# Kernel tuning notes

Hardware: AMD Instinct MI355X
Metric: run time of the kernel (lower is better)

The kernel has to match this reference:

```python
import jax, jax.numpy as jnp
import numpy as np

L = 4          # num_layers
DIM = 256      # model dim
HEADS = 8
DH = DIM // HEADS
WINDOW = 512   # sliding window size
FF = 4 * DIM
EPS = 1e-5


def setup_inputs() -> dict:
    key = jax.random.key(0)
    ks = jax.random.split(key, 13)
    B, S = 1, 4096
    s = 0.02
    inp = {
        "x": jax.random.normal(ks[0], (B, S, DIM), jnp.float32),
        # per-layer stacked weights (leading axis = layer) for lax.scan
        "wq": jax.random.normal(ks[1], (L, DIM, DIM), jnp.float32) * s,
        "bq": jnp.zeros((L, DIM), jnp.float32),
        "wk": jax.random.normal(ks[2], (L, DIM, DIM), jnp.float32) * s,
        "bk": jnp.zeros((L, DIM), jnp.float32),
        "wv": jax.random.normal(ks[3], (L, DIM, DIM), jnp.float32) * s,
        "bv": jnp.zeros((L, DIM), jnp.float32),
        "wo": jax.random.normal(ks[4], (L, DIM, DIM), jnp.float32) * s,
        "bo": jnp.zeros((L, DIM), jnp.float32),
        "w1": jax.random.normal(ks[5], (L, DIM, FF), jnp.float32) * s,
        "b1": jnp.zeros((L, FF), jnp.float32),
        "w2": jax.random.normal(ks[6], (L, FF, DIM), jnp.float32) * s,
        "b2": jnp.zeros((L, DIM), jnp.float32),
    }
    return inp


def _ln(x):
    # LayerNorm with elementwise_affine=False
    m = jnp.mean(x, axis=-1, keepdims=True)
    v = jnp.var(x, axis=-1, keepdims=True)
    return (x - m) / jnp.sqrt(v + EPS)


def reference(x, wq, bq, wk, bk, wv, bv, wo, bo, w1, b1, w2, b2):
    B, S, D = x.shape
    idx = jnp.arange(S)
    # sliding window mask: |q_idx - kv_idx| <= window_size // 2
    mask = jnp.abs(idx[:, None] - idx[None, :]) <= (WINDOW // 2)  # [S, S]
    neg = jnp.finfo(x.dtype).min
    scale = 1.0 / np.sqrt(DH)

    def layer(h, p):
        lwq, lbq, lwk, lbk, lwv, lbv, lwo, lbo, lw1, lb1, lw2, lb2 = p
        # pre-norm self-attention residual
        n = _ln(h)
        q = (n @ lwq + lbq).reshape(B, S, HEADS, DH)
        k = (n @ lwk + lbk).reshape(B, S, HEADS, DH)
        v = (n @ lwv + lbv).reshape(B, S, HEADS, DH)
        scores = jnp.einsum('bqhd,bkhd->bhqk', q, k) * scale
        scores = jnp.where(mask, scores, neg)
        attn = jax.nn.softmax(scores, axis=-1)
        o = jnp.einsum('bhqk,bkhd->bqhd', attn, v).reshape(B, S, D)
        h = h + o @ lwo + lbo
        # post-norm dense residual: x = norm(x); x = x + ffn(x)
        h = _ln(h)
        h = h + jax.nn.gelu(h @ lw1 + lb1) @ lw2 + lb2
        return h, None

    x, _ = jax.lax.scan(layer, x, (wq, bq, wk, bk, wv, bv, wo, bo, w1, b1, w2, b2))
    return x
```

## Files before the change

### kernel.cpp

```cpp
#include <hip/hip_runtime.h>
#include <math.h>

#define SEQ 4096
#define DIM 256
#define NH 8
#define DHD 32
#define FFD 1024
#define NLAYER 4

typedef unsigned short ushort_t;
typedef __attribute__((ext_vector_type(8))) short bf16x8;
typedef __attribute__((ext_vector_type(4))) float f32x4;

__device__ __forceinline__ float gelu_f(float x){
  const float c = 0.7978845608028654f;
  float x3 = x*x*x;
  return 0.5f * x * (1.0f + tanhf(c*(x + 0.044715f*x3)));
}

__device__ __forceinline__ ushort_t f2b(float f){
  union { float f; unsigned u; } x; x.f = f;
  unsigned r = x.u + 0x7FFF + ((x.u >> 16) & 1);
  return (ushort_t)(r >> 16);
}

__device__ __forceinline__ void gload16(void* lds, const void* g){
  __builtin_amdgcn_global_load_lds((const __attribute__((address_space(1))) void*)g,
                                   (__attribute__((address_space(3))) void*)lds, 16, 0, 0);
}

__global__ __launch_bounds__(256) void wconv_kernel(
    const float* __restrict__ wq, const float* __restrict__ wk,
    const float* __restrict__ wv, const float* __restrict__ wo,
    const float* __restrict__ w1, const float* __restrict__ w2,
    ushort_t* __restrict__ wt){
  __shared__ ushort_t tile[64][65];
  int b = blockIdx.x, tid = threadIdx.x;
  const float* src; ushort_t* dst; int K, N, tk, tn;
  if (b < 256){
    int m = b>>6, rem = b&63, l = rem>>4, t = rem&15;
    K = 256; N = 256; tk = t>>2; tn = t&3;
    const float* s4 = (m==0)?wq:(m==1)?wk:(m==2)?wv:wo;
    src = s4 + (size_t)l*65536;
    dst = wt + (size_t)(m*NLAYER + l)*65536;
  } else if (b < 512){
    int rem = b-256, l = rem>>6, t = rem&63;
    K = 256; N = 1024; tk = t>>4; tn = t&15;
    src = w1 + (size_t)l*262144;
    dst = wt + 1048576 + (size_t)l*262144;
  } else {
    int rem = b-512, l = rem>>6, t = rem&63;
    K = 1024; N = 256; tk = t>>2; tn = t&3;
    src = w2 + (size_t)l*262144;
    dst = wt + 2097152 + (size_t)l*262144;
  }
  int k0 = tk*64, n0 = tn*64;
  #pragma unroll
  for (int i=0;i<16;i++){
    int idx = tid + 256*i, row = idx>>6, col = idx&63;
    tile[row][col] = f2b(src[(size_t)(k0+row)*N + n0+col]);
  }
  __syncthreads();
  #pragma unroll
  for (int i=0;i<16;i++){
    int idx = tid + 256*i, nrow = idx>>6, kcol = idx&63;
    dst[(size_t)(n0+nrow)*K + k0+kcol] = tile[kcol][nrow];
  }
}

__global__ __launch_bounds__(256) void ln_kernel(const float* __restrict__ x,
    float* __restrict__ yf, ushort_t* __restrict__ yb){
  int row  = blockIdx.x*4 + (threadIdx.x>>6);
  int lane = threadIdx.x & 63;
  const float4* xr = (const float4*)(x + (size_t)row*DIM);
  float4 v = xr[lane];
  float s  = v.x+v.y+v.z+v.w;
  float sq = v.x*v.x+v.y*v.y+v.z*v.z+v.w*v.w;
  #pragma unroll
  for(int off=32; off>0; off>>=1){
    s  += __shfl_down(s, off);
    sq += __shfl_down(sq, off);
  }
  s = __shfl(s, 0); sq = __shfl(sq, 0);
  float mean = s * (1.0f/DIM);
  float var  = sq * (1.0f/DIM) - mean*mean;
  float rinv = rsqrtf(var + 1e-5f);
  float4 o;
  o.x=(v.x-mean)*rinv; o.y=(v.y-mean)*rinv; o.z=(v.z-mean)*rinv; o.w=(v.w-mean)*rinv;
  if (yf) ((float4*)(yf + (size_t)row*DIM))[lane] = o;
  if (yb){
    ushort_t* yp = yb + (size_t)row*DIM + lane*4;
    yp[0]=f2b(o.x); yp[1]=f2b(o.y); yp[2]=f2b(o.z); yp[3]=f2b(o.w);
  }
}

__global__ __launch_bounds__(256) void gemm_kernel(
    const ushort_t* __restrict__ A, const ushort_t* __restrict__ Wt,
    const float* __restrict__ bias, const float* __restrict__ R,
    float* __restrict__ Cf, ushort_t* __restrict__ Cb,
    int M, int N, int K, int act){
  __shared__ ushort_t As[32*256];
  __shared__ ushort_t Bs[64*256];
  int tid = threadIdx.x;
  int w = tid>>6, lane = tid&63;
  int wr = w>>1, wc = w&1;
  int q4 = lane>>4, u = lane&15;
  int m0 = blockIdx.y*32, n0 = blockIdx.x*64;
  f32x4 acc[2];
  acc[0] = (f32x4){0.f,0.f,0.f,0.f};
  acc[1] = (f32x4){0.f,0.f,0.f,0.f};

  for (int k0 = 0; k0 < K; k0 += 256){
    if (k0) __syncthreads();
    #pragma unroll
    for (int i=0;i<4;i++){
      int idx = tid + 256*i;
      int row = idx>>5, ch = idx&31;
      gload16(&As[idx*8], &A[(size_t)(m0+row)*K + k0 + ((ch^(row&7))*8)]);
    }
    #pragma unroll
    for (int i=0;i<8;i++){
      int idx = tid + 256*i;
      int row = idx>>5, ch = idx&31;
      gload16(&Bs[idx*8], &Wt[(size_t)(n0+row)*K + k0 + ((ch^(row&7))*8)]);
    }
    __syncthreads();
    #pragma unroll
    for (int kk=0;kk<8;kk++){
      int ar = wr*16 + u;
      bf16x8 af = *(const bf16x8*)&As[ar*256 + (((kk*4+q4)^(ar&7))*8)];
      #pragma unroll
      for (int j=0;j<2;j++){
        int br = wc*32 + j*16 + u;
        bf16x8 bf = *(const bf16x8*)&Bs[br*256 + (((kk*4+q4)^(br&7))*8)];
        acc[j] = __builtin_amdgcn_mfma_f32_16x16x32_bf16(af, bf, acc[j], 0, 0, 0);
      }
    }
  }
  #pragma unroll
  for (int j=0;j<2;j++){
    #pragma unroll
    for (int t=0;t<4;t++){
      int m = m0 + wr*16 + q4*4 + t;
      int n = n0 + wc*32 + j*16 + u;
      float val = acc[j][t] + bias[n];
      if (R)   val += R[(size_t)m*N + n];
      if (act) val = gelu_f(val);
      if (Cf)  Cf[(size_t)m*N + n] = val;
      if (Cb)  Cb[(size_t)m*N + n] = f2b(val);
    }
  }
}

__global__ __launch_bounds__(256) void qkv_kernel(
    const float* __restrict__ hin,
    const ushort_t* __restrict__ wtq, const ushort_t* __restrict__ wtk, const ushort_t* __restrict__ wtv,
    const float* __restrict__ bqp, const float* __restrict__ bkp, const float* __restrict__ bvp,
    ushort_t* __restrict__ qo, ushort_t* __restrict__ ko, ushort_t* __restrict__ vo){
  __shared__ ushort_t As[32*256];
  __shared__ ushort_t Bs[64*256];
  int tid = threadIdx.x;
  int w = tid>>6, lane = tid&63;
  int wr = w>>1, wc = w&1;
  int q4 = lane>>4, u = lane&15;
  int m0 = blockIdx.y*32, n0 = blockIdx.x*64;
  int z = blockIdx.z;
  const ushort_t* Wt = (z==0)?wtq:(z==1)?wtk:wtv;
  const float* bias  = (z==0)?bqp:(z==1)?bkp:bvp;
  ushort_t* Cb       = (z==0)?qo :(z==1)?ko :vo;

  #pragma unroll
  for (int i=0;i<8;i++){
    int idx = tid + 256*i;
    int row = idx>>5, ch = idx&31;
    gload16(&Bs[idx*8], &Wt[(size_t)(n0+row)*DIM + ((ch^(row&7))*8)]);
  }
  #pragma unroll
  for (int r=0;r<8;r++){
    int row = w*8 + r;
    float4 v = *(const float4*)&hin[(size_t)(m0+row)*DIM + lane*4];
    float s  = v.x+v.y+v.z+v.w;
    float sq = v.x*v.x+v.y*v.y+v.z*v.z+v.w*v.w;
    #pragma unroll
    for (int off=32; off>0; off>>=1){ s += __shfl_down(s,off); sq += __shfl_down(sq,off); }
    s = __shfl(s,0); sq = __shfl(sq,0);
    float mean = s*(1.0f/DIM), var = sq*(1.0f/DIM) - mean*mean;
    float rinv = rsqrtf(var + 1e-5f);
    int ch = lane>>1, half = lane&1;
    ushort4 o4;
    o4.x = f2b((v.x-mean)*rinv); o4.y = f2b((v.y-mean)*rinv);
    o4.z = f2b((v.z-mean)*rinv); o4.w = f2b((v.w-mean)*rinv);
    *(ushort4*)&As[row*256 + ((ch^(row&7))*8 + half*4)] = o4;
  }
  __syncthreads();

  f32x4 acc[2];
  acc[0] = (f32x4){0.f,0.f,0.f,0.f};
  acc[1] = (f32x4){0.f,0.f,0.f,0.f};
  #pragma unroll
  for (int kk=0;kk<8;kk++){
    int ar = wr*16 + u;
    bf16x8 af = *(const bf16x8*)&As[ar*256 + (((kk*4+q4)^(ar&7))*8)];
    #pragma unroll
    for (int j=0;j<2;j++){
      int br = wc*32 + j*16 + u;
      bf16x8 bf = *(const bf16x8*)&Bs[br*256 + (((kk*4+q4)^(br&7))*8)];
      acc[j] = __builtin_amdgcn_mfma_f32_16x16x32_bf16(af, bf, acc[j], 0, 0, 0);
    }
  }
  #pragma unroll
  for (int j=0;j<2;j++){
    #pragma unroll
    for (int t=0;t<4;t++){
      int m = m0 + wr*16 + q4*4 + t;
      int n = n0 + wc*32 + j*16 + u;
      Cb[(size_t)m*DIM + n] = f2b(acc[j][t] + bias[n]);
    }
  }
}

__global__ __launch_bounds__(256) void attn_kernel(
    const ushort_t* __restrict__ q, const ushort_t* __restrict__ k,
    const ushort_t* __restrict__ v, ushort_t* __restrict__ out){
  int q0 = blockIdx.x * 64;
  int h  = blockIdx.y;
  int tid = threadIdx.x;
  int w = tid >> 6;
  int lane = tid & 63;
  int u = lane & 15, q4 = lane >> 4;

  __shared__ ushort_t Ks[64][40];
  __shared__ ushort_t Vt[32][72];
  __shared__ ushort_t Pw[4][16][72];

  bf16x8 aq = *(const bf16x8*)(q + (size_t)(q0 + w*16 + u)*DIM + h*DHD + q4*8);

  float m[4], l[4];
  f32x4 acc[2];
  #pragma unroll
  for (int t=0;t<4;t++){ m[t] = -INFINITY; l[t] = 0.f; }
  acc[0] = (f32x4){0.f,0.f,0.f,0.f};
  acc[1] = (f32x4){0.f,0.f,0.f,0.f};

  const float sl2 = 0.25510703448358519f;

  int lo = q0 - 256; if (lo < 0) lo = 0;
  int hi = q0 + 63 + 256; if (hi > SEQ-1) hi = SEQ-1;
  int kt1 = (hi >> 6) << 6;

  for (int kt = (lo >> 6) << 6; kt <= kt1; kt += 64){
    __syncthreads();
    {
      int key = tid >> 2, d0 = (tid & 3) * 8;
      bf16x8 kv = *(const bf16x8*)(k + (size_t)(kt+key)*DIM + h*DHD + d0);
      *(bf16x8*)&Ks[key][d0] = kv;
      int vd0 = w * 8;
      bf16x8 vv = *(const bf16x8*)(v + (size_t)(kt+lane)*DIM + h*DHD + vd0);
      #pragma unroll
      for (int j=0;j<8;j++) Vt[vd0+j][lane] = (ushort_t)vv[j];
    }
    __syncthreads();

    f32x4 sc[4];
    #pragma unroll
    for (int t4=0;t4<4;t4++){
      bf16x8 bk = *(const bf16x8*)&Ks[t4*16 + u][q4*8];
      sc[t4] = __builtin_amdgcn_mfma_f32_16x16x32_bf16(aq, bk, (f32x4){0.f,0.f,0.f,0.f}, 0, 0, 0);
    }

    bool needs_mask = (kt < q0-192) || (kt > q0+192);
    #pragma unroll
    for (int t=0;t<4;t++){
      float mx = -INFINITY;
      if (needs_mask){
        int q_idx = q0 + w*16 + q4*4 + t;
        #pragma unroll
        for (int t4=0;t4<4;t4++){
          float s = sc[t4][t] * sl2;
          int k_idx = kt + t4*16 + u;
          int diff = q_idx - k_idx; if (diff < 0) diff = -diff;
          if (diff > 256) s = -INFINITY;
          sc[t4][t] = s;
          mx = fmaxf(mx, s);
        }
      } else {
        #pragma unroll
        for (int t4=0;t4<4;t4++){
          float s = sc[t4][t] * sl2;
          sc[t4][t] = s;
          mx = fmaxf(mx, s);
        }
      }
      mx = fmaxf(mx, __shfl_xor(mx, 1));
      mx = fmaxf(mx, __shfl_xor(mx, 2));
      mx = fmaxf(mx, __shfl_xor(mx, 4));
      mx = fmaxf(mx, __shfl_xor(mx, 8));
      float nm = fmaxf(m[t], mx);
      float al = exp2f(m[t] - nm);
      float rs = 0.f;
      #pragma unroll
      for (int t4=0;t4<4;t4++){
        float p = exp2f(sc[t4][t] - nm);
        rs += p;
        Pw[w][q4*4+t][t4*16+u] = f2b(p);
      }
      rs += __shfl_xor(rs, 1);
      rs += __shfl_xor(rs, 2);
      rs += __shfl_xor(rs, 4);
      rs += __shfl_xor(rs, 8);
      l[t] = l[t]*al + rs;
      m[t] = nm;
      acc[0][t] *= al;
      acc[1][t] *= al;
    }
    #pragma unroll
    for (int kk=0;kk<2;kk++){
      bf16x8 ap = *(const bf16x8*)&Pw[w][u][kk*32 + q4*8];
      #pragma unroll
      for (int d=0; d<2; d++){
        bf16x8 bvf = *(const bf16x8*)&Vt[d*16 + u][kk*32 + q4*8];
        acc[d] = __builtin_amdgcn_mfma_f32_16x16x32_bf16(ap, bvf, acc[d], 0, 0, 0);
      }
    }
  }

  float rl[4];
  #pragma unroll
  for (int t=0;t<4;t++) rl[t] = 1.0f / l[t];
  #pragma unroll
  for (int d=0; d<2; d++)
    #pragma unroll
    for (int t=0;t<4;t++)
      out[(size_t)(q0 + w*16 + q4*4 + t)*DIM + h*DHD + d*16 + u] = f2b(acc[d][t]*rl[t]);
}

extern "C" void kernel_launch(void* const* d_in, const int* in_sizes, int n_in,
                              void* d_out, int out_size, void* d_ws, size_t ws_size,
                              hipStream_t stream) {
  const float* x  = (const float*)d_in[0];
  const float* wq = (const float*)d_in[1];
  const float* bq = (const float*)d_in[2];
  const float* wk = (const float*)d_in[3];
  const float* bk = (const float*)d_in[4];
  const float* wv = (const float*)d_in[5];
  const float* bv = (const float*)d_in[6];
  const float* wo = (const float*)d_in[7];
  const float* bo = (const float*)d_in[8];
  const float* w1 = (const float*)d_in[9];
  const float* b1 = (const float*)d_in[10];
  const float* w2 = (const float*)d_in[11];
  const float* b2 = (const float*)d_in[12];
  float* out = (float*)d_out;
  float* ws  = (float*)d_ws;

  ushort_t* wt    = (ushort_t*)ws;
  ushort_t* abuf  = (ushort_t*)(ws + 1572864);
  ushort_t* ffbf  = (ushort_t*)(ws + 2097152);
  float* qb = ws + 4194304;
  float* kb = ws + 5242880;
  float* vb = ws + 6291456;
  float* hb = ws + 7340032;
  ushort_t* qbh = (ushort_t*)qb;
  ushort_t* kbh = (ushort_t*)kb;
  ushort_t* vbh = (ushort_t*)vb;

  const ushort_t* w1t_base = wt + 1048576;
  const ushort_t* w2t_base = wt + 2097152;

  const dim3 blk(256);
  wconv_kernel<<<768, blk, 0, stream>>>(wq, wk, wv, wo, w1, w2, wt);

  for (int l = 0; l < NLAYER; l++){
    const float* hin = (l == 0) ? x : hb;
    const ushort_t* lwq = wt + (size_t)(0*NLAYER + l)*65536;
    const ushort_t* lwk = wt + (size_t)(1*NLAYER + l)*65536;
    const ushort_t* lwv = wt + (size_t)(2*NLAYER + l)*65536;
    const ushort_t* lwo = wt + (size_t)(3*NLAYER + l)*65536;
    const ushort_t* lw1 = w1t_base + (size_t)l*262144;
    const ushort_t* lw2 = w2t_base + (size_t)l*262144;

    qkv_kernel<<<dim3(4,128,3), blk, 0, stream>>>(hin, lwq, lwk, lwv,
        bq + (size_t)l*DIM, bk + (size_t)l*DIM, bv + (size_t)l*DIM, qbh, kbh, vbh);
    attn_kernel<<<dim3(SEQ/64, NH), blk, 0, stream>>>(qbh, kbh, vbh, abuf);
    gemm_kernel<<<dim3(4,128), blk, 0, stream>>>(abuf, lwo, bo + (size_t)l*DIM,
        hin, qb, nullptr, SEQ, DIM, DIM, 0);
    ln_kernel<<<SEQ/4, blk, 0, stream>>>(qb, kb, abuf);
    gemm_kernel<<<dim3(16,128), blk, 0, stream>>>(abuf, lw1, b1 + (size_t)l*FFD,
        nullptr, nullptr, ffbf, SEQ, FFD, DIM, 1);
    float* hout = (l == NLAYER-1) ? out : hb;
    gemm_kernel<<<dim3(4,128), blk, 0, stream>>>(ffbf, lw2, b2 + (size_t)l*DIM,
        kb, hout, nullptr, SEQ, DIM, FFD, 0);
  }
}
```

Measured before the change: 381.0 us.

## Enlarge GEMM M-tile, fuse QKV per block, double-buffer attention K/V tiles

The GEMM and QKV kernels now compute 64x64 output tiles with a 2x2 MFMA accumulator block per wave, which halves the grid and improves register-level reuse of the A and B fragments. The QKV kernel computes the LayerNorm once per block and loops over the Q, K and V weights, reloading the B tile into shared memory between them instead of launching three z-slices. The attention kernel double-buffers its K/V shared tiles, prefetching the next tile into registers during compute and dropping one barrier per iteration. In exchange the kernels use more LDS and registers and launch fewer blocks, which may reduce occupancy and parallelism.

```diff
diff --git a/kernel.cpp b/kernel.cpp
--- a/kernel.cpp
+++ b/kernel.cpp
@@ -99,21 +99,24 @@
     const float* __restrict__ bias, const float* __restrict__ R,
     float* __restrict__ Cf, ushort_t* __restrict__ Cb,
     int M, int N, int K, int act){
-  __shared__ ushort_t As[32*256];
+  __shared__ ushort_t As[64*256];
   __shared__ ushort_t Bs[64*256];
   int tid = threadIdx.x;
   int w = tid>>6, lane = tid&63;
   int wr = w>>1, wc = w&1;
   int q4 = lane>>4, u = lane&15;
-  int m0 = blockIdx.y*32, n0 = blockIdx.x*64;
-  f32x4 acc[2];
-  acc[0] = (f32x4){0.f,0.f,0.f,0.f};
-  acc[1] = (f32x4){0.f,0.f,0.f,0.f};
+  int m0 = blockIdx.y*64, n0 = blockIdx.x*64;
+  f32x4 acc[2][2];
+  #pragma unroll
+  for (int i=0;i<2;i++)
+    #pragma unroll
+    for (int j=0;j<2;j++)
+      acc[i][j] = (f32x4){0.f,0.f,0.f,0.f};
 
   for (int k0 = 0; k0 < K; k0 += 256){
     if (k0) __syncthreads();
     #pragma unroll
-    for (int i=0;i<4;i++){
+    for (int i=0;i<8;i++){
       int idx = tid + 256*i;
       int row = idx>>5, ch = idx&31;
       gload16(&As[idx*8], &A[(size_t)(m0+row)*K + k0 + ((ch^(row&7))*8)]);
@@ -127,27 +130,38 @@
     __syncthreads();
     #pragma unroll
     for (int kk=0;kk<8;kk++){
-      int ar = wr*16 + u;
-      bf16x8 af = *(const bf16x8*)&As[ar*256 + (((kk*4+q4)^(ar&7))*8)];
+      bf16x8 af[2], bf[2];
+      #pragma unroll
+      for (int i=0;i<2;i++){
+        int ar = wr*32 + i*16 + u;
+        af[i] = *(const bf16x8*)&As[ar*256 + (((kk*4+q4)^(ar&7))*8)];
+      }
       #pragma unroll
       for (int j=0;j<2;j++){
         int br = wc*32 + j*16 + u;
-        bf16x8 bf = *(const bf16x8*)&Bs[br*256 + (((kk*4+q4)^(br&7))*8)];
-        acc[j] = __builtin_amdgcn_mfma_f32_16x16x32_bf16(af, bf, acc[j], 0, 0, 0);
-      }
-    }
-  }
-  #pragma unroll
-  for (int j=0;j<2;j++){
-    #pragma unroll
-    for (int t=0;t<4;t++){
-      int m = m0 + wr*16 + q4*4 + t;
-      int n = n0 + wc*32 + j*16 + u;
-      float val = acc[j][t] + bias[n];
-      if (R)   val += R[(size_t)m*N + n];
-      if (act) val = gelu_f(val);
-      if (Cf)  Cf[(size_t)m*N + n] = val;
-      if (Cb)  Cb[(size_t)m*N + n] = f2b(val);
+        bf[j] = *(const bf16x8*)&Bs[br*256 + (((kk*4+q4)^(br&7))*8)];
+      }
+      #pragma unroll
+      for (int i=0;i<2;i++)
+        #pragma unroll
+        for (int j=0;j<2;j++)
+          acc[i][j] = __builtin_amdgcn_mfma_f32_16x16x32_bf16(af[i], bf[j], acc[i][j], 0, 0, 0);
+    }
+  }
+  #pragma unroll
+  for (int i=0;i<2;i++){
+    #pragma unroll
+    for (int j=0;j<2;j++){
+      #pragma unroll
+      for (int t=0;t<4;t++){
+        int m = m0 + wr*32 + i*16 + q4*4 + t;
+        int n = n0 + wc*32 + j*16 + u;
+        float val = acc[i][j][t] + bias[n];
+        if (R)   val += R[(size_t)m*N + n];
+        if (act) val = gelu_f(val);
+        if (Cf)  Cf[(size_t)m*N + n] = val;
+        if (Cb)  Cb[(size_t)m*N + n] = f2b(val);
+      }
     }
   }
 }
@@ -157,27 +171,23 @@
     const ushort_t* __restrict__ wtq, const ushort_t* __restrict__ wtk, const ushort_t* __restrict__ wtv,
     const float* __restrict__ bqp, const float* __restrict__ bkp, const float* __restrict__ bvp,
     ushort_t* __restrict__ qo, ushort_t* __restrict__ ko, ushort_t* __restrict__ vo){
-  __shared__ ushort_t As[32*256];
+  __shared__ ushort_t As[64*256];
   __shared__ ushort_t Bs[64*256];
   int tid = threadIdx.x;
   int w = tid>>6, lane = tid&63;
   int wr = w>>1, wc = w&1;
   int q4 = lane>>4, u = lane&15;
-  int m0 = blockIdx.y*32, n0 = blockIdx.x*64;
-  int z = blockIdx.z;
-  const ushort_t* Wt = (z==0)?wtq:(z==1)?wtk:wtv;
-  const float* bias  = (z==0)?bqp:(z==1)?bkp:bvp;
-  ushort_t* Cb       = (z==0)?qo :(z==1)?ko :vo;
+  int m0 = blockIdx.y*64, n0 = blockIdx.x*64;
 
   #pragma unroll
   for (int i=0;i<8;i++){
     int idx = tid + 256*i;
     int row = idx>>5, ch = idx&31;
-    gload16(&Bs[idx*8], &Wt[(size_t)(n0+row)*DIM + ((ch^(row&7))*8)]);
-  }
-  #pragma unroll
-  for (int r=0;r<8;r++){
-    int row = w*8 + r;
+    gload16(&Bs[idx*8], &wtq[(size_t)(n0+row)*DIM + ((ch^(row&7))*8)]);
+  }
+  #pragma unroll
+  for (int r=0;r<16;r++){
+    int row = w*16 + r;
     float4 v = *(const float4*)&hin[(size_t)(m0+row)*DIM + lane*4];
     float s  = v.x+v.y+v.z+v.w;
     float sq = v.x*v.x+v.y*v.y+v.z*v.z+v.w*v.w;
@@ -194,28 +204,56 @@
   }
   __syncthreads();
 
-  f32x4 acc[2];
-  acc[0] = (f32x4){0.f,0.f,0.f,0.f};
-  acc[1] = (f32x4){0.f,0.f,0.f,0.f};
-  #pragma unroll
-  for (int kk=0;kk<8;kk++){
-    int ar = wr*16 + u;
-    bf16x8 af = *(const bf16x8*)&As[ar*256 + (((kk*4+q4)^(ar&7))*8)];
-    #pragma unroll
-    for (int j=0;j<2;j++){
-      int br = wc*32 + j*16 + u;
-      bf16x8 bf = *(const bf16x8*)&Bs[br*256 + (((kk*4+q4)^(br&7))*8)];
-      acc[j] = __builtin_amdgcn_mfma_f32_16x16x32_bf16(af, bf, acc[j], 0, 0, 0);
-    }
-  }
-  #pragma unroll
-  for (int j=0;j<2;j++){
-    #pragma unroll
-    for (int t=0;t<4;t++){
-      int m = m0 + wr*16 + q4*4 + t;
-      int n = n0 + wc*32 + j*16 + u;
-      Cb[(size_t)m*DIM + n] = f2b(acc[j][t] + bias[n]);
-    }
+  #pragma unroll
+  for (int z=0; z<3; z++){
+    const float* bias = (z==0)?bqp:(z==1)?bkp:bvp;
+    ushort_t* Cb      = (z==0)?qo :(z==1)?ko :vo;
+    f32x4 acc[2][2];
+    #pragma unroll
+    for (int i=0;i<2;i++)
+      #pragma unroll
+      for (int j=0;j<2;j++)
+        acc[i][j] = (f32x4){0.f,0.f,0.f,0.f};
+    #pragma unroll
+    for (int kk=0;kk<8;kk++){
+      bf16x8 af[2], bf[2];
+      #pragma unroll
+      for (int i=0;i<2;i++){
+        int ar = wr*32 + i*16 + u;
+        af[i] = *(const bf16x8*)&As[ar*256 + (((kk*4+q4)^(ar&7))*8)];
+      }
+      #pragma unroll
+      for (int j=0;j<2;j++){
+        int br = wc*32 + j*16 + u;
+        bf[j] = *(const bf16x8*)&Bs[br*256 + (((kk*4+q4)^(br&7))*8)];
+      }
+      #pragma unroll
+      for (int i=0;i<2;i++)
+        #pragma unroll
+        for (int j=0;j<2;j++)
+          acc[i][j] = __builtin_amdgcn_mfma_f32_16x16x32_bf16(af[i], bf[j], acc[i][j], 0, 0, 0);
+    }
+    if (z < 2){
+      __syncthreads();
+      const ushort_t* Wn = (z==0)?wtk:wtv;
+      #pragma unroll
+      for (int i=0;i<8;i++){
+        int idx = tid + 256*i;
+        int row = idx>>5, ch = idx&31;
+        gload16(&Bs[idx*8], &Wn[(size_t)(n0+row)*DIM + ((ch^(row&7))*8)]);
+      }
+    }
+    #pragma unroll
+    for (int i=0;i<2;i++)
+      #pragma unroll
+      for (int j=0;j<2;j++)
+        #pragma unroll
+        for (int t=0;t<4;t++){
+          int m = m0 + wr*32 + i*16 + q4*4 + t;
+          int n = n0 + wc*32 + j*16 + u;
+          Cb[(size_t)m*DIM + n] = f2b(acc[i][j][t] + bias[n]);
+        }
+    if (z < 2) __syncthreads();
   }
 }
 
@@ -229,8 +267,8 @@
   int lane = tid & 63;
   int u = lane & 15, q4 = lane >> 4;
 
-  __shared__ ushort_t Ks[64][40];
-  __shared__ ushort_t Vt[32][72];
+  __shared__ ushort_t Ks[2][64][40];
+  __shared__ ushort_t Vt[2][32][72];
   __shared__ ushort_t Pw[4][16][72];
 
   bf16x8 aq = *(const bf16x8*)(q + (size_t)(q0 + w*16 + u)*DIM + h*DHD + q4*8);
@@ -246,25 +284,31 @@
 
   int lo = q0 - 256; if (lo < 0) lo = 0;
   int hi = q0 + 63 + 256; if (hi > SEQ-1) hi = SEQ-1;
+  int kt0 = (lo >> 6) << 6;
   int kt1 = (hi >> 6) << 6;
 
-  for (int kt = (lo >> 6) << 6; kt <= kt1; kt += 64){
+  int key = tid >> 2, d0 = (tid & 3) * 8;
+  int vd0 = w * 8;
+
+  bf16x8 kr = *(const bf16x8*)(k + (size_t)(kt0+key)*DIM + h*DHD + d0);
+  bf16x8 vr = *(const bf16x8*)(v + (size_t)(kt0+lane)*DIM + h*DHD + vd0);
+  *(bf16x8*)&Ks[0][key][d0] = kr;
+  #pragma unroll
+  for (int j=0;j<8;j++) Vt[0][vd0+j][lane] = (ushort_t)vr[j];
+
+  int p = 0;
+  for (int kt = kt0; kt <= kt1; kt += 64, p ^= 1){
     __syncthreads();
-    {
-      int key = tid >> 2, d0 = (tid & 3) * 8;
-      bf16x8 kv = *(const bf16x8*)(k + (size_t)(kt+key)*DIM + h*DHD + d0);
-      *(bf16x8*)&Ks[key][d0] = kv;
-      int vd0 = w * 8;
-      bf16x8 vv = *(const bf16x8*)(v + (size_t)(kt+lane)*DIM + h*DHD + vd0);
-      #pragma unroll
-      for (int j=0;j<8;j++) Vt[vd0+j][lane] = (ushort_t)vv[j];
-    }
-    __syncthreads();
+    bool have_next = (kt + 64 <= kt1);
+    if (have_next){
+      kr = *(const bf16x8*)(k + (size_t)(kt+64+key)*DIM + h*DHD + d0);
+      vr = *(const bf16x8*)(v + (size_t)(kt+64+lane)*DIM + h*DHD + vd0);
+    }
 
     f32x4 sc[4];
     #pragma unroll
     for (int t4=0;t4<4;t4++){
-      bf16x8 bk = *(const bf16x8*)&Ks[t4*16 + u][q4*8];
+      bf16x8 bk = *(const bf16x8*)&Ks[p][t4*16 + u][q4*8];
       sc[t4] = __builtin_amdgcn_mfma_f32_16x16x32_bf16(aq, bk, (f32x4){0.f,0.f,0.f,0.f}, 0, 0, 0);
     }
 
@@ -300,9 +344,9 @@
       float rs = 0.f;
       #pragma unroll
       for (int t4=0;t4<4;t4++){
-        float p = exp2f(sc[t4][t] - nm);
-        rs += p;
-        Pw[w][q4*4+t][t4*16+u] = f2b(p);
+        float pv = exp2f(sc[t4][t] - nm);
+        rs += pv;
+        Pw[w][q4*4+t][t4*16+u] = f2b(pv);
       }
       rs += __shfl_xor(rs, 1);
       rs += __shfl_xor(rs, 2);
@@ -318,9 +362,14 @@
       bf16x8 ap = *(const bf16x8*)&Pw[w][u][kk*32 + q4*8];
       #pragma unroll
       for (int d=0; d<2; d++){
-        bf16x8 bvf = *(const bf16x8*)&Vt[d*16 + u][kk*32 + q4*8];
+        bf16x8 bvf = *(const bf16x8*)&Vt[p][d*16 + u][kk*32 + q4*8];
         acc[d] = __builtin_amdgcn_mfma_f32_16x16x32_bf16(ap, bvf, acc[d], 0, 0, 0);
       }
+    }
+    if (have_next){
+      *(bf16x8*)&Ks[p^1][key][d0] = kr;
+      #pragma unroll
+      for (int j=0;j<8;j++) Vt[p^1][vd0+j][lane] = (ushort_t)vr[j];
     }
   }
 
@@ -379,16 +428,16 @@
     const ushort_t* lw1 = w1t_base + (size_t)l*262144;
     const ushort_t* lw2 = w2t_base + (size_t)l*262144;
 
-    qkv_kernel<<<dim3(4,128,3), blk, 0, stream>>>(hin, lwq, lwk, lwv,
+    qkv_kernel<<<dim3(4,64), blk, 0, stream>>>(hin, lwq, lwk, lwv,
         bq + (size_t)l*DIM, bk + (size_t)l*DIM, bv + (size_t)l*DIM, qbh, kbh, vbh);
     attn_kernel<<<dim3(SEQ/64, NH), blk, 0, stream>>>(qbh, kbh, vbh, abuf);
-    gemm_kernel<<<dim3(4,128), blk, 0, stream>>>(abuf, lwo, bo + (size_t)l*DIM,
+    gemm_kernel<<<dim3(4,64), blk, 0, stream>>>(abuf, lwo, bo + (size_t)l*DIM,
         hin, qb, nullptr, SEQ, DIM, DIM, 0);
     ln_kernel<<<SEQ/4, blk, 0, stream>>>(qb, kb, abuf);
-    gemm_kernel<<<dim3(16,128), blk, 0, stream>>>(abuf, lw1, b1 + (size_t)l*FFD,
+    gemm_kernel<<<dim3(16,64), blk, 0, stream>>>(abuf, lw1, b1 + (size_t)l*FFD,
         nullptr, nullptr, ffbf, SEQ, FFD, DIM, 1);
     float* hout = (l == NLAYER-1) ? out : hb;
-    gemm_kernel<<<dim3(4,128), blk, 0, stream>>>(ffbf, lw2, b2 + (size_t)l*DIM,
+    gemm_kernel<<<dim3(4,64), blk, 0, stream>>>(ffbf, lw2, b2 + (size_t)l*DIM,
         kb, hout, nullptr, SEQ, DIM, FFD, 0);
   }
 }
```

New measurement: 385.7 us. Within noise of the previous version (+1.2%).

## Reuse normalized A tile across Q/K/V and double-buffer K/V tiles in attention

Applied to the files above, without the earlier changes.

The QKV kernel now computes the LayerNorm'd activation tile once per block and loops over the three weight matrices, reloading only the B tile, instead of launching three z-slices that each redo the LN. The attention kernel double-buffers K and V in shared memory, prefetching the next tile into registers while computing on the current one, which removes one barrier per iteration. The cost is fewer QKV blocks (less parallelism), extra serialized weight loads within each block, and more shared memory in attention, which may lower occupancy.

```diff
diff --git a/kernel.cpp b/kernel.cpp
--- a/kernel.cpp
+++ b/kernel.cpp
@@ -164,16 +164,12 @@
   int wr = w>>1, wc = w&1;
   int q4 = lane>>4, u = lane&15;
   int m0 = blockIdx.y*32, n0 = blockIdx.x*64;
-  int z = blockIdx.z;
-  const ushort_t* Wt = (z==0)?wtq:(z==1)?wtk:wtv;
-  const float* bias  = (z==0)?bqp:(z==1)?bkp:bvp;
-  ushort_t* Cb       = (z==0)?qo :(z==1)?ko :vo;
 
   #pragma unroll
   for (int i=0;i<8;i++){
     int idx = tid + 256*i;
     int row = idx>>5, ch = idx&31;
-    gload16(&Bs[idx*8], &Wt[(size_t)(n0+row)*DIM + ((ch^(row&7))*8)]);
+    gload16(&Bs[idx*8], &wtq[(size_t)(n0+row)*DIM + ((ch^(row&7))*8)]);
   }
   #pragma unroll
   for (int r=0;r<8;r++){
@@ -194,28 +190,42 @@
   }
   __syncthreads();
 
-  f32x4 acc[2];
-  acc[0] = (f32x4){0.f,0.f,0.f,0.f};
-  acc[1] = (f32x4){0.f,0.f,0.f,0.f};
-  #pragma unroll
-  for (int kk=0;kk<8;kk++){
-    int ar = wr*16 + u;
-    bf16x8 af = *(const bf16x8*)&As[ar*256 + (((kk*4+q4)^(ar&7))*8)];
-    #pragma unroll
-    for (int j=0;j<2;j++){
-      int br = wc*32 + j*16 + u;
-      bf16x8 bf = *(const bf16x8*)&Bs[br*256 + (((kk*4+q4)^(br&7))*8)];
-      acc[j] = __builtin_amdgcn_mfma_f32_16x16x32_bf16(af, bf, acc[j], 0, 0, 0);
-    }
-  }
-  #pragma unroll
-  for (int j=0;j<2;j++){
-    #pragma unroll
-    for (int t=0;t<4;t++){
-      int m = m0 + wr*16 + q4*4 + t;
-      int n = n0 + wc*32 + j*16 + u;
-      Cb[(size_t)m*DIM + n] = f2b(acc[j][t] + bias[n]);
-    }
+  #pragma unroll
+  for (int z=0; z<3; z++){
+    const float* bias = (z==0)?bqp:(z==1)?bkp:bvp;
+    ushort_t* Cb      = (z==0)?qo :(z==1)?ko :vo;
+    f32x4 acc[2];
+    acc[0]=(f32x4){0.f,0.f,0.f,0.f}; acc[1]=(f32x4){0.f,0.f,0.f,0.f};
+    #pragma unroll
+    for (int kk=0;kk<8;kk++){
+      int ar = wr*16 + u;
+      bf16x8 af = *(const bf16x8*)&As[ar*256 + (((kk*4+q4)^(ar&7))*8)];
+      #pragma unroll
+      for (int j=0;j<2;j++){
+        int br = wc*32 + j*16 + u;
+        bf16x8 bf = *(const bf16x8*)&Bs[br*256 + (((kk*4+q4)^(br&7))*8)];
+        acc[j] = __builtin_amdgcn_mfma_f32_16x16x32_bf16(af, bf, acc[j], 0, 0, 0);
+      }
+    }
+    if (z < 2){
+      __syncthreads();
+      const ushort_t* Wn = (z==0)?wtk:wtv;
+      #pragma unroll
+      for (int i=0;i<8;i++){
+        int idx = tid + 256*i;
+        int row = idx>>5, ch = idx&31;
+        gload16(&Bs[idx*8], &Wn[(size_t)(n0+row)*DIM + ((ch^(row&7))*8)]);
+      }
+    }
+    #pragma unroll
+    for (int j=0;j<2;j++)
+      #pragma unroll
+      for (int t=0;t<4;t++){
+        int m = m0 + wr*16 + q4*4 + t;
+        int n = n0 + wc*32 + j*16 + u;
+        Cb[(size_t)m*DIM + n] = f2b(acc[j][t] + bias[n]);
+      }
+    if (z < 2) __syncthreads();
   }
 }
 
@@ -229,8 +239,8 @@
   int lane = tid & 63;
   int u = lane & 15, q4 = lane >> 4;
 
-  __shared__ ushort_t Ks[64][40];
-  __shared__ ushort_t Vt[32][72];
+  __shared__ ushort_t Ks[2][64][40];
+  __shared__ ushort_t Vt[2][32][72];
   __shared__ ushort_t Pw[4][16][72];
 
   bf16x8 aq = *(const bf16x8*)(q + (size_t)(q0 + w*16 + u)*DIM + h*DHD + q4*8);
@@ -246,25 +256,31 @@
 
   int lo = q0 - 256; if (lo < 0) lo = 0;
   int hi = q0 + 63 + 256; if (hi > SEQ-1) hi = SEQ-1;
+  int kt0 = (lo >> 6) << 6;
   int kt1 = (hi >> 6) << 6;
 
-  for (int kt = (lo >> 6) << 6; kt <= kt1; kt += 64){
+  int key = tid >> 2, d0 = (tid & 3) * 8;
+  int vd0 = w * 8;
+
+  bf16x8 kr = *(const bf16x8*)(k + (size_t)(kt0+key)*DIM + h*DHD + d0);
+  bf16x8 vr = *(const bf16x8*)(v + (size_t)(kt0+lane)*DIM + h*DHD + vd0);
+  *(bf16x8*)&Ks[0][key][d0] = kr;
+  #pragma unroll
+  for (int j=0;j<8;j++) Vt[0][vd0+j][lane] = (ushort_t)vr[j];
+
+  int p = 0;
+  for (int kt = kt0; kt <= kt1; kt += 64, p ^= 1){
     __syncthreads();
-    {
-      int key = tid >> 2, d0 = (tid & 3) * 8;
-      bf16x8 kv = *(const bf16x8*)(k + (size_t)(kt+key)*DIM + h*DHD + d0);
-      *(bf16x8*)&Ks[key][d0] = kv;
-      int vd0 = w * 8;
-      bf16x8 vv = *(const bf16x8*)(v + (size_t)(kt+lane)*DIM + h*DHD + vd0);
-      #pragma unroll
-      for (int j=0;j<8;j++) Vt[vd0+j][lane] = (ushort_t)vv[j];
-    }
-    __syncthreads();
+    bool have_next = (kt + 64 <= kt1);
+    if (have_next){
+      kr = *(const bf16x8*)(k + (size_t)(kt+64+key)*DIM + h*DHD + d0);
+      vr = *(const bf16x8*)(v + (size_t)(kt+64+lane)*DIM + h*DHD + vd0);
+    }
 
     f32x4 sc[4];
     #pragma unroll
     for (int t4=0;t4<4;t4++){
-      bf16x8 bk = *(const bf16x8*)&Ks[t4*16 + u][q4*8];
+      bf16x8 bk = *(const bf16x8*)&Ks[p][t4*16 + u][q4*8];
       sc[t4] = __builtin_amdgcn_mfma_f32_16x16x32_bf16(aq, bk, (f32x4){0.f,0.f,0.f,0.f}, 0, 0, 0);
     }
 
@@ -300,9 +316,9 @@
       float rs = 0.f;
       #pragma unroll
       for (int t4=0;t4<4;t4++){
-        float p = exp2f(sc[t4][t] - nm);
-        rs += p;
-        Pw[w][q4*4+t][t4*16+u] = f2b(p);
+        float pv = exp2f(sc[t4][t] - nm);
+        rs += pv;
+        Pw[w][q4*4+t][t4*16+u] = f2b(pv);
       }
       rs += __shfl_xor(rs, 1);
       rs += __shfl_xor(rs, 2);
@@ -318,9 +334,14 @@
       bf16x8 ap = *(const bf16x8*)&Pw[w][u][kk*32 + q4*8];
       #pragma unroll
       for (int d=0; d<2; d++){
-        bf16x8 bvf = *(const bf16x8*)&Vt[d*16 + u][kk*32 + q4*8];
+        bf16x8 bvf = *(const bf16x8*)&Vt[p][d*16 + u][kk*32 + q4*8];
         acc[d] = __builtin_amdgcn_mfma_f32_16x16x32_bf16(ap, bvf, acc[d], 0, 0, 0);
       }
+    }
+    if (have_next){
+      *(bf16x8*)&Ks[p^1][key][d0] = kr;
+      #pragma unroll
+      for (int j=0;j<8;j++) Vt[p^1][vd0+j][lane] = (ushort_t)vr[j];
     }
   }
 
@@ -379,7 +400,7 @@
     const ushort_t* lw1 = w1t_base + (size_t)l*262144;
     const ushort_t* lw2 = w2t_base + (size_t)l*262144;
 
-    qkv_kernel<<<dim3(4,128,3), blk, 0, stream>>>(hin, lwq, lwk, lwv,
+    qkv_kernel<<<dim3(4,128), blk, 0, stream>>>(hin, lwq, lwk, lwv,
         bq + (size_t)l*DIM, bk + (size_t)l*DIM, bv + (size_t)l*DIM, qbh, kbh, vbh);
     attn_kernel<<<dim3(SEQ/64, NH), blk, 0, stream>>>(qbh, kbh, vbh, abuf);
     gemm_kernel<<<dim3(4,128), blk, 0, stream>>>(abuf, lwo, bo + (size_t)l*DIM,
```

New measurement: 360.5 us. -5.4%, faster.
